# Optimization experiments

Hardware: AMD Instinct MI355X
Metric: run time of the kernel (lower is better)

The kernel has to match this reference:

```python
import jax, jax.numpy as jnp
import numpy as np

DELTA = 0.1625
FREQ_SCALE = 0.325
MIN_LAYERS = 1
MAX_LAYERS = 5
EPS = 1e-12  # F.normalize eps


def _l2norm(x, axis):
    n = jnp.sqrt(jnp.sum(x * x, axis=axis, keepdims=True))
    return x / jnp.maximum(n, EPS)


def setup_inputs() -> dict:
    key = jax.random.key(0)
    k1, k2, k3 = jax.random.split(key, 3)
    B, N, D = 8, 2048, 64
    embeddings = jax.random.normal(k1, (B, N, D), dtype=jnp.float32)
    # scale to [0, 15) so echo_layers spans the full 1..5 range
    frequencies = jax.random.uniform(k2, (B, N), dtype=jnp.float32) * 15.0
    relationship_matrix = jax.random.uniform(k3, (B, N, N), dtype=jnp.float32)
    return {"embeddings": embeddings, "frequencies": frequencies,
            "relationship_matrix": relationship_matrix}


def reference(embeddings, frequencies, relationship_matrix):
    B, N, D = embeddings.shape
    # per-token number of echo iterations
    echo_layers = jnp.clip(
        MIN_LAYERS + jnp.floor(frequencies * FREQ_SCALE), MIN_LAYERS, MAX_LAYERS
    ).astype(jnp.int32)  # [B, N]

    refined = _l2norm(embeddings, axis=2)  # [B, N, D]

    # mask out the diagonal of the relationship matrix once (it is constant
    # across layers); shifts[i] = delta * sum_j rm[i,j]*(e_i - e_j)
    #               = delta * (e_i * rowsum[i] - (rm @ e)[i])
    rm = relationship_matrix * (1.0 - jnp.eye(N, dtype=relationship_matrix.dtype))
    rowsum = jnp.sum(rm, axis=-1)  # [B, N]

    def step(e, layer):
        active = (layer < echo_layers)[..., None].astype(e.dtype)  # [B, N, 1]
        agg = jnp.einsum('bij,bjd->bid', rm, e)                     # [B, N, D]
        shifts = DELTA * (e * rowsum[..., None] - agg)
        upd = _l2norm(e + shifts * active, axis=2)
        # tokens with zero shift are already unit-norm, so renorm is identity
        return upd, None

    refined, _ = jax.lax.scan(step, refined, jnp.arange(MAX_LAYERS))
    return refined
```

## Files before the change

kernel.cpp:

```cpp
#include <hip/hip_runtime.h>
#include <stdint.h>

#define BB 8
#define NN 2048
#define DD 64
#define DELTA 0.1625f
#define FREQ_SCALE 0.325f

typedef __bf16 bf16x8 __attribute__((ext_vector_type(8)));
typedef float f32x4 __attribute__((ext_vector_type(4)));
typedef unsigned int u32x4 __attribute__((ext_vector_type(4)));
typedef unsigned int u32x2 __attribute__((ext_vector_type(2)));

static __device__ __forceinline__ unsigned short f2b(float x) {
    union { float f; unsigned int u; } c; c.f = x;
    unsigned int r = (c.u + 0x7FFFu + ((c.u >> 16) & 1u)) >> 16;
    return (unsigned short)r;
}

static __device__ __forceinline__ void gl_lds16(const void* g, void* l) {
    __builtin_amdgcn_global_load_lds(
        (const __attribute__((address_space(1))) void*)g,
        (__attribute__((address_space(3))) void*)l, 16, 0, 0);
}

__global__ __launch_bounds__(256) void prep_norm(
        const float* __restrict__ emb, const float* __restrict__ freq,
        float* __restrict__ e0, unsigned short* __restrict__ eT0,
        int* __restrict__ echo) {
    __shared__ unsigned short tile[64][72];
    int t = threadIdx.x;
    int tok0 = blockIdx.x * 64;
    int lt = t >> 2;
    int tt = tok0 + lt;
    int dd = (t & 3) * 16;

    const float* src = emb + (size_t)tt * DD + dd;
    f32x4 v[4];
    float ss = 0.f;
    #pragma unroll
    for (int q = 0; q < 4; q++) {
        v[q] = *(const f32x4*)(src + q * 4);
        ss += v[q].x*v[q].x + v[q].y*v[q].y + v[q].z*v[q].z + v[q].w*v[q].w;
    }
    ss += __shfl_xor(ss, 1);
    ss += __shfl_xor(ss, 2);
    float scale = 1.f / fmaxf(sqrtf(ss), 1e-12f);
    float* dst = e0 + (size_t)tt * DD + dd;
    #pragma unroll
    for (int q = 0; q < 4; q++) {
        f32x4 o = v[q] * scale;
        *(f32x4*)(dst + q * 4) = o;
        tile[lt][dd + q*4 + 0] = f2b(o.x);
        tile[lt][dd + q*4 + 1] = f2b(o.y);
        tile[lt][dd + q*4 + 2] = f2b(o.z);
        tile[lt][dd + q*4 + 3] = f2b(o.w);
    }
    if ((t & 3) == 0) {
        int el = 1 + (int)floorf(freq[tt] * FREQ_SCALE);
        el = el < 1 ? 1 : (el > 5 ? 5 : el);
        echo[tt] = el;
    }
    __syncthreads();
    int b  = tok0 / NN;
    int tb = tok0 % NN;
    for (int idx = t; idx < 64 * 64; idx += 256) {
        int d = idx >> 6, j = idx & 63;
        eT0[((size_t)b * DD + d) * NN + tb + j] = tile[j][d];
    }
}

template<bool WRB>
__global__ __launch_bounds__(256) void cast_rowsum(
        const float* __restrict__ rm, unsigned short* __restrict__ rmb,
        float* __restrict__ rowsum) {
    int gw = (int)((blockIdx.x * 256 + threadIdx.x) >> 6);
    int l = threadIdx.x & 63;
    const float* src = rm + (size_t)gw * NN;
    f32x4 v[8];
    #pragma unroll
    for (int q = 0; q < 8; q++)
        v[q] = *(const f32x4*)(src + q * 256 + l * 4);
    float s = 0.f;
    #pragma unroll
    for (int q = 0; q < 8; q++)
        s += (v[q].x + v[q].y) + (v[q].z + v[q].w);
    if constexpr (WRB) {
        unsigned short* dst = rmb + (size_t)gw * NN;
        #pragma unroll
        for (int q = 0; q < 8; q++) {
            u32x2 o;
            o.x = (unsigned)f2b(v[q].x) | ((unsigned)f2b(v[q].y) << 16);
            o.y = (unsigned)f2b(v[q].z) | ((unsigned)f2b(v[q].w) << 16);
            *(u32x2*)(dst + q * 256 + l * 4) = o;
        }
    }
    #pragma unroll
    for (int m = 1; m < 64; m <<= 1) s += __shfl_xor(s, m);
    if (l == 0) rowsum[gw] = s;
}

__global__ __launch_bounds__(512, 1) void layer_fused(
        const unsigned short* __restrict__ rmb,
        const unsigned short* __restrict__ eT_src,
        const float* __restrict__ e_src,
        const float* __restrict__ rowsum_g,
        const int* __restrict__ echo,
        float* __restrict__ e_dst,
        unsigned short* __restrict__ eT_dst,
        int layer) {
    __shared__ char SB6[6][8192];
    __shared__ char SA6[6][8192];
    __shared__ float redSS[4][2][16];

    const int t = threadIdx.x;
    const int w = t >> 6, l = t & 63;
    const int lo = l & 15, hi = l >> 4;
    const int it = w & 3, dh = w >> 2;
    const int gid = blockIdx.x;
    const int b  = gid & 7;
    const int i0 = (gid >> 3) * 64;

    const char* rmB = (const char*)(rmb + ((size_t)b * NN + i0) * NN);
    const char* eTB = (const char*)(eT_src + (size_t)b * DD * NN);

    const size_t srow = (size_t)(w * 8 + (l >> 3)) * (NN * 2);
    const int csrc = ((l & 7) ^ (l >> 3)) << 4;

    f32x4 acc0 = {}, acc1 = {};

    const int rowB  = it * 16 + lo;
    const int rowA0 = dh * 32 + lo;
    const int rowA1 = dh * 32 + 16 + lo;
    const int xr = (lo & 7) << 4;

#define ISSUE(bi, step) do {                                       \
    const int ksb = (step) * 128;                                  \
    gl_lds16(rmB + srow + ksb + csrc, &SB6[bi][w * 1024]);         \
    gl_lds16(eTB + srow + ksb + csrc, &SA6[bi][w * 1024]);         \
} while (0)

#define COMP(bi) do {                                              \
    __builtin_amdgcn_s_setprio(1);                                 \
    _Pragma("unroll")                                              \
    for (int kk = 0; kk < 2; kk++) {                               \
        int co = ((kk << 6) | (hi << 4)) ^ xr;                     \
        u32x4 fB  = *(const u32x4*)(&SB6[bi][rowB  * 128 + co]);   \
        u32x4 fA0 = *(const u32x4*)(&SA6[bi][rowA0 * 128 + co]);   \
        u32x4 fA1 = *(const u32x4*)(&SA6[bi][rowA1 * 128 + co]);   \
        acc0 = __builtin_amdgcn_mfma_f32_16x16x32_bf16(            \
            __builtin_bit_cast(bf16x8, fA0), __builtin_bit_cast(bf16x8, fB), acc0, 0, 0, 0); \
        acc1 = __builtin_amdgcn_mfma_f32_16x16x32_bf16(            \
            __builtin_bit_cast(bf16x8, fA1), __builtin_bit_cast(bf16x8, fB), acc1, 0, 0, 0); \
    }                                                              \
    __builtin_amdgcn_s_setprio(0);                                 \
} while (0)

    ISSUE(0, 0);
    ISSUE(1, 1);
    ISSUE(2, 2);
    ISSUE(3, 3);
    ISSUE(4, 4);
    #pragma unroll
    for (int s = 0; s < 32; s++) {
        if (s < 29)       asm volatile("s_waitcnt vmcnt(8)" ::: "memory");
        else if (s == 29) asm volatile("s_waitcnt vmcnt(4)" ::: "memory");
        else if (s == 30) asm volatile("s_waitcnt vmcnt(2)" ::: "memory");
        else              asm volatile("s_waitcnt vmcnt(0)" ::: "memory");
        __builtin_amdgcn_s_barrier();
        __builtin_amdgcn_sched_barrier(0);
        if (s < 27) {
            const int nb = (s + 5) % 6;
            if (nb == 0)      ISSUE(0, s + 5);
            else if (nb == 1) ISSUE(1, s + 5);
            else if (nb == 2) ISSUE(2, s + 5);
            else if (nb == 3) ISSUE(3, s + 5);
            else if (nb == 4) ISSUE(4, s + 5);
            else              ISSUE(5, s + 5);
        }
        const int cb = s % 6;
        if (cb == 0)      COMP(0);
        else if (cb == 1) COMP(1);
        else if (cb == 2) COMP(2);
        else if (cb == 3) COMP(3);
        else if (cb == 4) COMP(4);
        else              COMP(5);
    }
#undef ISSUE
#undef COMP

    const size_t gi = (size_t)b * NN + i0 + it * 16 + lo;
    const float rs = rowsum_g[gi];
    const float coef = (layer < echo[gi]) ? DELTA : 0.f;
    const size_t eb = gi * DD + dh * 32 + hi * 4;
    f32x4 e0 = *(const f32x4*)(e_src + eb);
    f32x4 e1 = *(const f32x4*)(e_src + eb + 16);
    f32x4 u0 = e0 + coef * (e0 * rs - acc0);
    f32x4 u1 = e1 + coef * (e1 * rs - acc1);
    float ss = u0.x*u0.x + u0.y*u0.y + u0.z*u0.z + u0.w*u0.w
             + u1.x*u1.x + u1.y*u1.y + u1.z*u1.z + u1.w*u1.w;
    ss += __shfl_xor(ss, 16);
    ss += __shfl_xor(ss, 32);
    if (hi == 0) redSS[it][dh][lo] = ss;
    __syncthreads();
    float sst = redSS[it][0][lo] + redSS[it][1][lo];
    float scale = 1.f / fmaxf(sqrtf(sst), 1e-12f);
    u0 *= scale;
    u1 *= scale;
    *(f32x4*)(e_dst + eb) = u0;
    *(f32x4*)(e_dst + eb + 16) = u1;
    unsigned short* ep = eT_dst + (size_t)b * DD * NN;
    const int i = i0 + it * 16 + lo;
    const int d0 = dh * 32 + hi * 4;
    ep[(size_t)(d0 + 0)  * NN + i] = f2b(u0.x);
    ep[(size_t)(d0 + 1)  * NN + i] = f2b(u0.y);
    ep[(size_t)(d0 + 2)  * NN + i] = f2b(u0.z);
    ep[(size_t)(d0 + 3)  * NN + i] = f2b(u0.w);
    ep[(size_t)(d0 + 16) * NN + i] = f2b(u1.x);
    ep[(size_t)(d0 + 17) * NN + i] = f2b(u1.y);
    ep[(size_t)(d0 + 18) * NN + i] = f2b(u1.z);
    ep[(size_t)(d0 + 19) * NN + i] = f2b(u1.w);
}

__global__ __launch_bounds__(512, 4) void layer_step_fb(
        const float* __restrict__ rm_,
        const unsigned short* __restrict__ eT_src,
        const float* __restrict__ e_src,
        const float* __restrict__ rowsum_g,
        const int* __restrict__ echo,
        float* __restrict__ e_dst,
        unsigned short* __restrict__ eT_dst,
        int layer) {
    __shared__ float redAcc[3][2][64][20];

    int t = threadIdx.x;
    int w = t >> 6, l = t & 63;
    int b = blockIdx.y;
    int i0 = blockIdx.x * 32;
    int wi = w & 1;
    int kq = w >> 1;
    int lane_lo = l & 15, lane_hi = l >> 4;
    int i = i0 + wi * 16 + lane_lo;
    size_t gi = (size_t)b * NN + i;
    int kbase = kq * (NN / 4) + 8 * lane_hi;

    int echo_pre = echo[gi];
    float rs = rowsum_g[gi];

    const unsigned short* eT_b = eT_src + (size_t)b * DD * NN;
    const unsigned short* ea0 = eT_b + (size_t)(lane_lo)      * NN + kbase;
    const unsigned short* ea1 = eT_b + (size_t)(16 + lane_lo) * NN + kbase;
    const unsigned short* ea2 = eT_b + (size_t)(32 + lane_lo) * NN + kbase;
    const unsigned short* ea3 = eT_b + (size_t)(48 + lane_lo) * NN + kbase;

    f32x4 acc[4] = {};
    const float* rmp32 = rm_ + gi * NN + kbase;

    #pragma unroll
    for (int j = 0; j < 16; j++) {
        const int o = 32 * j;
        f32x4 lo4 = *(const f32x4*)(rmp32 + o);
        f32x4 hi4 = *(const f32x4*)(rmp32 + o + 4);
        u32x4 ob;
        ob.x = (unsigned)f2b(lo4.x) | ((unsigned)f2b(lo4.y) << 16);
        ob.y = (unsigned)f2b(lo4.z) | ((unsigned)f2b(lo4.w) << 16);
        ob.z = (unsigned)f2b(hi4.x) | ((unsigned)f2b(hi4.y) << 16);
        ob.w = (unsigned)f2b(hi4.z) | ((unsigned)f2b(hi4.w) << 16);
        bf16x8 bfrag = __builtin_bit_cast(bf16x8, ob);
        acc[0] = __builtin_amdgcn_mfma_f32_16x16x32_bf16(
            __builtin_bit_cast(bf16x8, *(const u32x4*)(ea0 + o)), bfrag, acc[0], 0, 0, 0);
        acc[1] = __builtin_amdgcn_mfma_f32_16x16x32_bf16(
            __builtin_bit_cast(bf16x8, *(const u32x4*)(ea1 + o)), bfrag, acc[1], 0, 0, 0);
        acc[2] = __builtin_amdgcn_mfma_f32_16x16x32_bf16(
            __builtin_bit_cast(bf16x8, *(const u32x4*)(ea2 + o)), bfrag, acc[2], 0, 0, 0);
        acc[3] = __builtin_amdgcn_mfma_f32_16x16x32_bf16(
            __builtin_bit_cast(bf16x8, *(const u32x4*)(ea3 + o)), bfrag, acc[3], 0, 0, 0);
    }

    if (kq > 0) {
        #pragma unroll
        for (int f = 0; f < 4; f++)
            *(f32x4*)(&redAcc[kq - 1][wi][l][4 * f]) = acc[f];
    }
    __syncthreads();
    if (kq == 0) {
        #pragma unroll
        for (int f = 0; f < 4; f++) {
            acc[f] += *(const f32x4*)(&redAcc[0][wi][l][4 * f]);
            acc[f] += *(const f32x4*)(&redAcc[1][wi][l][4 * f]);
            acc[f] += *(const f32x4*)(&redAcc[2][wi][l][4 * f]);
        }
        float coef = DELTA * ((layer < echo_pre) ? 1.f : 0.f);
        size_t ebase = gi * DD;
        f32x4 upd[4];
        float ss = 0.f;
        #pragma unroll
        for (int f = 0; f < 4; f++) {
            f32x4 e = *(const f32x4*)(e_src + ebase + 16 * f + 4 * lane_hi);
            f32x4 u = e + coef * (e * rs - acc[f]);
            upd[f] = u;
            ss += u.x*u.x + u.y*u.y + u.z*u.z + u.w*u.w;
        }
        ss += __shfl_xor(ss, 16);
        ss += __shfl_xor(ss, 32);
        float scale = 1.f / fmaxf(sqrtf(ss), 1e-12f);
        unsigned short* ep = eT_dst + (size_t)b * DD * NN;
        #pragma unroll
        for (int f = 0; f < 4; f++) {
            f32x4 o = upd[f] * scale;
            *(f32x4*)(e_dst + ebase + 16 * f + 4 * lane_hi) = o;
            int dbase = 16 * f + 4 * lane_hi;
            ep[(size_t)(dbase + 0) * NN + i] = f2b(o.x);
            ep[(size_t)(dbase + 1) * NN + i] = f2b(o.y);
            ep[(size_t)(dbase + 2) * NN + i] = f2b(o.z);
            ep[(size_t)(dbase + 3) * NN + i] = f2b(o.w);
        }
    }
}

extern "C" void kernel_launch(void* const* d_in, const int* in_sizes, int n_in,
                              void* d_out, int out_size, void* d_ws, size_t ws_size,
                              hipStream_t stream) {
    const float* emb  = (const float*)d_in[0];
    const float* freq = (const float*)d_in[1];
    const float* rm   = (const float*)d_in[2];
    float* out = (float*)d_out;
    char* ws = (char*)d_ws;

    const size_t eBytes   = (size_t)BB * NN * DD * 4;
    const size_t eTBytes  = (size_t)BB * DD * NN * 2;
    const size_t bnBytes  = (size_t)BB * NN * 4;
    const size_t rmbBytes = (size_t)BB * NN * NN * 2;
    float* e_f32[2] = { (float*)ws, (float*)(ws + eBytes) };
    unsigned short* eT[2] = { (unsigned short*)(ws + 2*eBytes),
                              (unsigned short*)(ws + 2*eBytes + eTBytes) };
    float* rowsum = (float*)(ws + 2*eBytes + 2*eTBytes);
    int* echo = (int*)(ws + 2*eBytes + 2*eTBytes + bnBytes);
    unsigned short* rmb = (unsigned short*)(ws + 2*eBytes + 2*eTBytes + 2*bnBytes);
    size_t need_cached = 2*eBytes + 2*eTBytes + 2*bnBytes + rmbBytes;

    int cached = (ws_size >= need_cached) ? 1 : 0;

    prep_norm<<<dim3(BB*NN/64), dim3(256), 0, stream>>>(emb, freq, e_f32[0], eT[0], echo);

    if (cached) {
        cast_rowsum<true><<<dim3(BB*NN/4), dim3(256), 0, stream>>>(rm, rmb, rowsum);
        for (int l = 0; l < 5; l++) {
            float* dst = (l == 4) ? out : e_f32[(l + 1) & 1];
            layer_fused<<<dim3(256), dim3(512), 0, stream>>>(
                rmb, eT[l & 1], e_f32[l & 1], rowsum, echo,
                dst, eT[(l + 1) & 1], l);
        }
    } else {
        cast_rowsum<false><<<dim3(BB*NN/4), dim3(256), 0, stream>>>(rm, nullptr, rowsum);
        for (int l = 0; l < 5; l++) {
            float* dst = (l == 4) ? out : e_f32[(l + 1) & 1];
            layer_step_fb<<<dim3(NN/32, BB), dim3(512), 0, stream>>>(
                rm, eT[l & 1], e_f32[l & 1], rowsum, echo,
                dst, eT[(l + 1) & 1], l);
        }
    }
}
```

Before: 119.3 us.

## Fuse fp32-to-bf16 cast and rowsum into first layer GEMM kernel

Replaces the separate cast_rowsum pass plus the first layer_fused launch with a single kernel. It streams the fp32 relationship matrix into LDS, converts it to bf16, writes the bf16 copy to global memory, and accumulates row sums. The converted tile is then fed straight into the MFMA for layer 0. This removes one full fp32 read of the matrix and a bf16 re-read, plus one launch. In exchange, layer 0 becomes a more complex pipeline with larger fp32 tiles in LDS and a hand-tuned waitcnt schedule.

```diff
diff --git a/kernel.cpp b/kernel.cpp
--- a/kernel.cpp
+++ b/kernel.cpp
@@ -98,6 +98,169 @@
     #pragma unroll
     for (int m = 1; m < 64; m <<= 1) s += __shfl_xor(s, m);
     if (l == 0) rowsum[gw] = s;
+}
+
+__global__ __launch_bounds__(512, 1) void layer0_fused(
+        const float* __restrict__ rm,
+        const unsigned short* __restrict__ eT_src,
+        const float* __restrict__ e_src,
+        const int* __restrict__ echo,
+        unsigned short* __restrict__ rmb_out,
+        float* __restrict__ rowsum_out,
+        float* __restrict__ e_dst,
+        unsigned short* __restrict__ eT_dst) {
+    __shared__ char F4[4][16384];
+    __shared__ char C4[4][8192];
+    __shared__ char SA4[4][8192];
+    __shared__ float redSS[4][2][16];
+    __shared__ float rsumL[64];
+
+    const int t = threadIdx.x;
+    const int w = t >> 6, l = t & 63;
+    const int lo = l & 15, hi = l >> 4;
+    const int it = w & 3, dh = w >> 2;
+    const int gid = blockIdx.x;
+    const int b  = gid & 7;
+    const int i0 = (gid >> 3) * 64;
+
+    const char* rmB = (const char*)(rm + ((size_t)b * NN + i0) * NN);
+    const char* eTB = (const char*)(eT_src + (size_t)b * DD * NN);
+
+    const size_t frow0 = (size_t)(w * 8 + (l >> 4)) * (NN * 4);
+    const size_t frow4 = (size_t)(w * 8 + 4 + (l >> 4)) * (NN * 4);
+    const int fcs0 = (((l & 15) ^ (l >> 4)) << 4);
+    const int fcs4 = (((l & 15) ^ (4 + (l >> 4))) << 4);
+    const size_t srowE = (size_t)(w * 8 + (l >> 3)) * (NN * 2);
+    const int csrcE = (((l & 7) ^ (l >> 3)) << 4);
+
+    const int rl = w * 8 + (l >> 3);
+    const int cs0 = ((2 * (l & 7)) ^ (l >> 3)) << 4;
+    const int cs1 = ((2 * (l & 7) + 1) ^ (l >> 3)) << 4;
+    const int cdst = rl * 128 + ((((l & 7) ^ (l >> 3))) << 4);
+    unsigned short* rmbW = rmb_out + ((size_t)b * NN + i0 + rl) * NN + (l & 7) * 8;
+
+    f32x4 acc0 = {}, acc1 = {};
+    float rsum = 0.f;
+
+    const int rowB  = it * 16 + lo;
+    const int rowA0 = dh * 32 + lo;
+    const int rowA1 = dh * 32 + 16 + lo;
+    const int xr = (lo & 7) << 4;
+
+#define ISSUE(bi, step) do {                                        \
+    const int kf = (step) * 256;                                    \
+    const int ke = (step) * 128;                                    \
+    gl_lds16(rmB + frow0 + kf + fcs0, &F4[bi][w * 2048]);           \
+    gl_lds16(rmB + frow4 + kf + fcs4, &F4[bi][w * 2048 + 1024]);    \
+    gl_lds16(eTB + srowE + ke + csrcE, &SA4[bi][w * 1024]);         \
+} while (0)
+
+#define CONVERT(bi, step) do {                                      \
+    f32x4 va = *(const f32x4*)(&F4[bi][rl * 256 + cs0]);            \
+    f32x4 vb = *(const f32x4*)(&F4[bi][rl * 256 + cs1]);            \
+    u32x4 o;                                                        \
+    o.x = (unsigned)f2b(va.x) | ((unsigned)f2b(va.y) << 16);        \
+    o.y = (unsigned)f2b(va.z) | ((unsigned)f2b(va.w) << 16);        \
+    o.z = (unsigned)f2b(vb.x) | ((unsigned)f2b(vb.y) << 16);        \
+    o.w = (unsigned)f2b(vb.z) | ((unsigned)f2b(vb.w) << 16);        \
+    *(u32x4*)(&C4[bi][cdst]) = o;                                   \
+    *(u32x4*)(rmbW + (step) * 64) = o;                              \
+    rsum += (va.x + va.y + va.z + va.w) + (vb.x + vb.y + vb.z + vb.w); \
+} while (0)
+
+#define COMP(bi) do {                                               \
+    __builtin_amdgcn_s_setprio(1);                                  \
+    _Pragma("unroll")                                               \
+    for (int kk = 0; kk < 2; kk++) {                                \
+        int co = ((kk << 6) | (hi << 4)) ^ xr;                      \
+        u32x4 fB  = *(const u32x4*)(&C4[bi][rowB  * 128 + co]);     \
+        u32x4 fA0 = *(const u32x4*)(&SA4[bi][rowA0 * 128 + co]);    \
+        u32x4 fA1 = *(const u32x4*)(&SA4[bi][rowA1 * 128 + co]);    \
+        acc0 = __builtin_amdgcn_mfma_f32_16x16x32_bf16(             \
+            __builtin_bit_cast(bf16x8, fA0), __builtin_bit_cast(bf16x8, fB), acc0, 0, 0, 0); \
+        acc1 = __builtin_amdgcn_mfma_f32_16x16x32_bf16(             \
+            __builtin_bit_cast(bf16x8, fA1), __builtin_bit_cast(bf16x8, fB), acc1, 0, 0, 0); \
+    }                                                               \
+    __builtin_amdgcn_s_setprio(0);                                  \
+} while (0)
+
+    ISSUE(0, 0);
+    ISSUE(1, 1);
+    ISSUE(2, 2);
+    #pragma unroll
+    for (int s = 0; s < 32; s++) {
+        if (s == 0)       asm volatile("s_waitcnt vmcnt(6)" ::: "memory");
+        else if (s == 1)  asm volatile("s_waitcnt vmcnt(7)" ::: "memory");
+        else if (s == 2)  asm volatile("s_waitcnt vmcnt(8)" ::: "memory");
+        else if (s < 30)  asm volatile("s_waitcnt vmcnt(9)" ::: "memory");
+        else if (s == 30) asm volatile("s_waitcnt vmcnt(6)" ::: "memory");
+        else              asm volatile("s_waitcnt vmcnt(3)" ::: "memory");
+        __builtin_amdgcn_s_barrier();
+        __builtin_amdgcn_sched_barrier(0);
+        if (s < 29) {
+            const int nb = (s + 3) & 3;
+            if (nb == 0)      ISSUE(0, s + 3);
+            else if (nb == 1) ISSUE(1, s + 3);
+            else if (nb == 2) ISSUE(2, s + 3);
+            else              ISSUE(3, s + 3);
+        }
+        const int cb = s & 3;
+        if (cb == 0)      CONVERT(0, s);
+        else if (cb == 1) CONVERT(1, s);
+        else if (cb == 2) CONVERT(2, s);
+        else              CONVERT(3, s);
+        asm volatile("s_waitcnt lgkmcnt(0)" ::: "memory");
+        __builtin_amdgcn_sched_barrier(0);
+        __builtin_amdgcn_s_barrier();
+        if (cb == 0)      COMP(0);
+        else if (cb == 1) COMP(1);
+        else if (cb == 2) COMP(2);
+        else              COMP(3);
+    }
+#undef ISSUE
+#undef CONVERT
+#undef COMP
+
+    rsum += __shfl_xor(rsum, 1);
+    rsum += __shfl_xor(rsum, 2);
+    rsum += __shfl_xor(rsum, 4);
+    if ((l & 7) == 0) {
+        rsumL[rl] = rsum;
+        rowsum_out[(size_t)b * NN + i0 + rl] = rsum;
+    }
+    __syncthreads();
+
+    const size_t gi = (size_t)b * NN + i0 + it * 16 + lo;
+    const float rs = rsumL[it * 16 + lo];
+    const float coef = (0 < echo[gi]) ? DELTA : 0.f;
+    const size_t eb = gi * DD + dh * 32 + hi * 4;
+    f32x4 e0 = *(const f32x4*)(e_src + eb);
+    f32x4 e1 = *(const f32x4*)(e_src + eb + 16);
+    f32x4 u0 = e0 + coef * (e0 * rs - acc0);
+    f32x4 u1 = e1 + coef * (e1 * rs - acc1);
+    float ss = u0.x*u0.x + u0.y*u0.y + u0.z*u0.z + u0.w*u0.w
+             + u1.x*u1.x + u1.y*u1.y + u1.z*u1.z + u1.w*u1.w;
+    ss += __shfl_xor(ss, 16);
+    ss += __shfl_xor(ss, 32);
+    if (hi == 0) redSS[it][dh][lo] = ss;
+    __syncthreads();
+    float sst = redSS[it][0][lo] + redSS[it][1][lo];
+    float scale = 1.f / fmaxf(sqrtf(sst), 1e-12f);
+    u0 *= scale;
+    u1 *= scale;
+    *(f32x4*)(e_dst + eb) = u0;
+    *(f32x4*)(e_dst + eb + 16) = u1;
+    unsigned short* ep = eT_dst + (size_t)b * DD * NN;
+    const int i = i0 + it * 16 + lo;
+    const int d0 = dh * 32 + hi * 4;
+    ep[(size_t)(d0 + 0)  * NN + i] = f2b(u0.x);
+    ep[(size_t)(d0 + 1)  * NN + i] = f2b(u0.y);
+    ep[(size_t)(d0 + 2)  * NN + i] = f2b(u0.z);
+    ep[(size_t)(d0 + 3)  * NN + i] = f2b(u0.w);
+    ep[(size_t)(d0 + 16) * NN + i] = f2b(u1.x);
+    ep[(size_t)(d0 + 17) * NN + i] = f2b(u1.y);
+    ep[(size_t)(d0 + 18) * NN + i] = f2b(u1.z);
+    ep[(size_t)(d0 + 19) * NN + i] = f2b(u1.w);
 }
 
 __global__ __launch_bounds__(512, 1) void layer_fused(
@@ -344,8 +507,9 @@
     prep_norm<<<dim3(BB*NN/64), dim3(256), 0, stream>>>(emb, freq, e_f32[0], eT[0], echo);
 
     if (cached) {
-        cast_rowsum<true><<<dim3(BB*NN/4), dim3(256), 0, stream>>>(rm, rmb, rowsum);
-        for (int l = 0; l < 5; l++) {
+        layer0_fused<<<dim3(256), dim3(512), 0, stream>>>(
+            rm, eT[0], e_f32[0], echo, rmb, rowsum, e_f32[1], eT[1]);
+        for (int l = 1; l < 5; l++) {
             float* dst = (l == 4) ? out : e_f32[(l + 1) & 1];
             layer_fused<<<dim3(256), dim3(512), 0, stream>>>(
                 rmb, eT[l & 1], e_f32[l & 1], rowsum, echo,
```

Result: faster. 106.7 us (median of 2 runs) (-10.5%).
